# Performance work log

Measured on AMD Instinct MI355X. Metric: run time of the kernel, lower is better.

## Reference

```python
import jax, jax.numpy as jnp
import numpy as np

D_MODEL = 768
N_HEADS = 12
HEAD = 64
B, T = 2, 2048


def setup_inputs() -> dict:
    key = jax.random.key(0)
    k1, k2, k3 = jax.random.split(key, 3)
    x = jax.random.normal(k1, (B, T, D_MODEL), dtype=jnp.float32)
    W1 = jax.random.normal(k2, (3 * D_MODEL, D_MODEL), dtype=jnp.float32) * (1.0 / np.sqrt(D_MODEL))
    b1 = jnp.zeros((3 * D_MODEL,), dtype=jnp.float32)
    W2 = jax.random.normal(k3, (D_MODEL, D_MODEL), dtype=jnp.float32) * (1.0 / np.sqrt(D_MODEL))
    b2 = jnp.zeros((D_MODEL,), dtype=jnp.float32)
    return {"x": x, "W1": W1, "b1": b1, "W2": W2, "b2": b2}


def reference(x, W1, b1, W2, b2):
    Bx, Tx, C = x.shape
    qkv = jnp.einsum('btc,fc->btf', x, W1) + b1            # (B,T,3C)
    q, k, v = jnp.split(qkv, 3, axis=-1)
    # (B,T,H,Dh) -> (B,H,T,Dh)
    q = q.reshape(Bx, Tx, N_HEADS, HEAD).transpose(0, 2, 1, 3)
    k = k.reshape(Bx, Tx, N_HEADS, HEAD).transpose(0, 2, 1, 3)
    v = v.reshape(Bx, Tx, N_HEADS, HEAD).transpose(0, 2, 1, 3)
    scale = 1.0 / np.sqrt(HEAD)
    scores = jnp.einsum('bhqd,bhkd->bhqk', q, k) * scale   # (B,H,T,T)
    causal = jnp.tril(jnp.ones((Tx, Tx), dtype=bool))
    scores = jnp.where(causal, scores, jnp.finfo(scores.dtype).min)
    attn = jax.nn.softmax(scores, axis=-1)
    o = jnp.einsum('bhqk,bhkd->bhqd', attn, v)             # (B,H,T,Dh)
    o = o.transpose(0, 2, 1, 3).reshape(Bx, Tx, C)
    return jnp.einsum('btc,fc->btf', o, W2) + b2
```

## Files before the change

### kernel.cpp

```cpp
#include <hip/hip_runtime.h>


typedef float f32x4 __attribute__((ext_vector_type(4)));
typedef __bf16 bf16x8 __attribute__((ext_vector_type(8)));
typedef unsigned int u32x4 __attribute__((ext_vector_type(4)));

#define D_MODEL 768
#define F3 2304
#define NHEADS 12
#define HEAD 64
#define BB 2
#define TT 2048
#define MROWS (BB*TT)
#define KDIM 768
#define LOG2E 1.44269504f
#define NX (MROWS*D_MODEL)
#define NW1 (F3*KDIM)
#define NW2 (D_MODEL*KDIM)
#define NHT 16
#define NOF (BB*NHEADS*NHT*64*64)
#define NLF (BB*NHEADS*NHT*64)

__device__ __forceinline__ unsigned short f2bf(float f) {
    unsigned int u = __float_as_uint(f);
    u += 0x7fffu + ((u >> 16) & 1u);
    return (unsigned short)(u >> 16);
}
__device__ __forceinline__ unsigned int pack2bf(float a, float b) {
    unsigned int ua = __float_as_uint(a), ub = __float_as_uint(b);
    ua += 0x7fffu + ((ua >> 16) & 1u);
    ub += 0x7fffu + ((ub >> 16) & 1u);
    return (ua >> 16) | (ub & 0xffff0000u);
}

__device__ __forceinline__ void async_copy16(unsigned short* lds, const unsigned short* g) {
    __builtin_amdgcn_global_load_lds(
        (const __attribute__((address_space(1))) unsigned int*)(const void*)g,
        (__attribute__((address_space(3))) unsigned int*)(void*)lds,
        16, 0, 0);
}

__global__ void prep(const float* __restrict__ x, const float* __restrict__ W1,
                     const float* __restrict__ W2, unsigned short* __restrict__ xb,
                     unsigned short* __restrict__ w1b, unsigned short* __restrict__ w2b) {
    const int i4 = (blockIdx.x * blockDim.x + threadIdx.x) * 4;
    const float* src; unsigned short* dst; int off;
    if (i4 < NX)                  { src = x;  dst = xb;  off = i4; }
    else if (i4 < NX + NW1)       { src = W1; dst = w1b; off = i4 - NX; }
    else if (i4 < NX + NW1 + NW2) { src = W2; dst = w2b; off = i4 - NX - NW1; }
    else return;
    float4 v = *(const float4*)(src + off);
    uint2 o;
    o.x = pack2bf(v.x, v.y);
    o.y = pack2bf(v.z, v.w);
    *(uint2*)(dst + off) = o;
}

__global__ __launch_bounds__(256, 4) void gemm1(
    const unsigned short* __restrict__ A, const unsigned short* __restrict__ Bw,
    const float* __restrict__ bias, int K,
    unsigned short* __restrict__ Qb, unsigned short* __restrict__ Kb,
    unsigned short* __restrict__ VT)
{
    __shared__ unsigned short As[128*64];
    __shared__ unsigned short Bs[96*64];
    const int tid  = threadIdx.x;
    const int wave = tid >> 6;
    const int lane = tid & 63;
    const int quad = lane >> 4;
    const int l16  = lane & 15;

    const int F   = blockIdx.x;
    const int xcd = F & 7;
    const int idx = F >> 3;
    const int bm  = (xcd & 3) * 8 + (idx & 7);
    const int bn  = (xcd >> 2) * 12 + (idx >> 3);
    const int m0  = bm * 128;
    const int n0  = bn * 96;
    const int seg = bn >> 3;

    const int wm = (wave >> 1) * 64;
    const int wn = (wave & 1) * 48;

    f32x4 acc[4][3] = {};

    const unsigned short* Ablk = A + (size_t)m0 * K;
    const unsigned short* Bblk = Bw + (size_t)n0 * K;
    const int srow = tid >> 3;
    const int scol = ((tid & 7) ^ (srow & 7)) * 8;

    for (int k0 = 0; k0 < K; k0 += 64) {
        #pragma unroll
        for (int r = 0; r < 4; ++r)
            async_copy16(As + r*2048 + tid*8,
                         Ablk + (size_t)(r*32 + srow) * K + k0 + scol);
        #pragma unroll
        for (int r = 0; r < 3; ++r)
            async_copy16(Bs + r*2048 + tid*8,
                         Bblk + (size_t)(r*32 + srow) * K + k0 + scol);
        asm volatile("s_waitcnt vmcnt(0)" ::: "memory");
        __syncthreads();

        #pragma unroll
        for (int kc2 = 0; kc2 < 2; ++kc2) {
            const int pos = ((kc2*4 + quad) ^ (l16 & 7)) * 8;
            bf16x8 a[4], b[3];
            #pragma unroll
            for (int i = 0; i < 4; ++i)
                a[i] = *(const bf16x8*)(As + (wm + i*16 + l16)*64 + pos);
            #pragma unroll
            for (int j = 0; j < 3; ++j)
                b[j] = *(const bf16x8*)(Bs + (wn + j*16 + l16)*64 + pos);
            #pragma unroll
            for (int i = 0; i < 4; ++i)
                #pragma unroll
                for (int j = 0; j < 3; ++j)
                    acc[i][j] = __builtin_amdgcn_mfma_f32_16x16x32_bf16(a[i], b[j], acc[i][j], 0, 0, 0);
        }
        __syncthreads();
    }

    if (seg < 2) {
        #pragma unroll
        for (int j = 0; j < 3; ++j) {
            const int n = n0 + wn + j*16 + l16;
            const float bv = bias[n];
            const int f = n - seg * 768;
            const int h = f >> 6, d = f & 63;
            #pragma unroll
            for (int i = 0; i < 4; ++i)
                #pragma unroll
                for (int r = 0; r < 4; ++r) {
                    const int m = m0 + wm + i*16 + quad*4 + r;
                    const int b = m >> 11, t = m & 2047;
                    const size_t idxq = (((size_t)(b*NHEADS + h)) * TT + t) * HEAD + d;
                    const float v = acc[i][j][r] + bv;
                    if (seg == 0) Qb[idxq] = f2bf(v * (0.125f * LOG2E));
                    else          Kb[idxq] = f2bf(v);
                }
        }
    } else {
        #pragma unroll
        for (int j = 0; j < 3; ++j) {
            const int n = n0 + wn + j*16 + l16;
            const float bv = bias[n];
            const int f = n - 1536;
            const int h = f >> 6, d = f & 63;
            #pragma unroll
            for (int i = 0; i < 4; ++i) {
                const int m = m0 + wm + i*16 + quad*4;
                const int b = m >> 11, t = m & 2047;
                uint2 pk;
                pk.x = pack2bf(acc[i][j][0] + bv, acc[i][j][1] + bv);
                pk.y = pack2bf(acc[i][j][2] + bv, acc[i][j][3] + bv);
                *(uint2*)(VT + ((size_t)(b*NHEADS + h) * HEAD + d) * TT + t) = pk;
            }
        }
    }
}

__global__ __launch_bounds__(256, 4) void gemm2(
    const unsigned short* __restrict__ A, const unsigned short* __restrict__ Bw,
    const float* __restrict__ bias, int K, float* __restrict__ Cout)
{
    __shared__ unsigned short As[64*64];
    __shared__ unsigned short Bs[96*64];
    const int tid  = threadIdx.x;
    const int wave = tid >> 6;
    const int lane = tid & 63;
    const int quad = lane >> 4;
    const int l16  = lane & 15;

    const int F   = blockIdx.x;
    const int xcd = F & 7;
    const int idx = F >> 3;
    const int m0  = ((xcd & 3) * 16 + (idx & 15)) * 64;
    const int n0  = ((xcd >> 2) * 4 + (idx >> 4)) * 96;

    const int wm = (wave >> 1) * 32;
    const int wn = (wave & 1) * 48;

    f32x4 acc[2][3] = {};

    const unsigned short* Ablk = A + (size_t)m0 * K;
    const unsigned short* Bblk = Bw + (size_t)n0 * K;
    const int srow = tid >> 3;
    const int scol = ((tid & 7) ^ (srow & 7)) * 8;

    for (int k0 = 0; k0 < K; k0 += 64) {
        #pragma unroll
        for (int r = 0; r < 2; ++r)
            async_copy16(As + r*2048 + tid*8,
                         Ablk + (size_t)(r*32 + srow) * K + k0 + scol);
        #pragma unroll
        for (int r = 0; r < 3; ++r)
            async_copy16(Bs + r*2048 + tid*8,
                         Bblk + (size_t)(r*32 + srow) * K + k0 + scol);
        asm volatile("s_waitcnt vmcnt(0)" ::: "memory");
        __syncthreads();

        #pragma unroll
        for (int kc2 = 0; kc2 < 2; ++kc2) {
            const int pos = ((kc2*4 + quad) ^ (l16 & 7)) * 8;
            bf16x8 a[2], b[3];
            #pragma unroll
            for (int i = 0; i < 2; ++i)
                a[i] = *(const bf16x8*)(As + (wm + i*16 + l16)*64 + pos);
            #pragma unroll
            for (int j = 0; j < 3; ++j)
                b[j] = *(const bf16x8*)(Bs + (wn + j*16 + l16)*64 + pos);
            #pragma unroll
            for (int i = 0; i < 2; ++i)
                #pragma unroll
                for (int j = 0; j < 3; ++j)
                    acc[i][j] = __builtin_amdgcn_mfma_f32_16x16x32_bf16(a[i], b[j], acc[i][j], 0, 0, 0);
        }
        __syncthreads();
    }

    #pragma unroll
    for (int j = 0; j < 3; ++j) {
        const int n = n0 + wn + j*16 + l16;
        const float bv = bias[n];
        #pragma unroll
        for (int i = 0; i < 2; ++i)
            #pragma unroll
            for (int r = 0; r < 4; ++r) {
                const int m = m0 + wm + i*16 + quad*4 + r;
                Cout[(size_t)m * D_MODEL + n] = acc[i][j][r] + bv;
            }
    }
}

__global__ __launch_bounds__(256, 4) void attn(
    const unsigned short* __restrict__ Qb, const unsigned short* __restrict__ Kb,
    const unsigned short* __restrict__ VT, unsigned short* __restrict__ Ob,
    float* __restrict__ OfA, float* __restrict__ OfB,
    float* __restrict__ LfA, float* __restrict__ LfB)
{
    __shared__ unsigned short Ks[128*64];
    __shared__ unsigned short Vt[64*128];

    const int tid  = threadIdx.x;
    const int wave = tid >> 6;
    const int lane = tid & 63;
    const int quad = lane >> 4;
    const int l16  = lane & 15;

    const int F    = blockIdx.y * 32 + blockIdx.x;
    const int xcd  = F & 7;
    const int slot = F >> 3;
    const int bh   = xcd * 3 + (slot >> 5);
    const int j    = slot & 31;

    const int i    = j & 15;
    const bool isA = (j < 16);
    const int half = i >> 1;
    const int split = 8 - half;
    const size_t hbase = (size_t)bh * TT * HEAD;

    const int krow = tid >> 3;
    const int kchunk = ((tid & 7) ^ (krow & 7)) * 8;
    const int vrow = tid >> 4;
    const int vchunk = ((tid & 15) ^ vrow) * 8;

    const int nseg = isA ? 2 : 1;
    for (int segi = 0; segi < nseg; ++segi) {
        int qt, kb, ke; bool full;
        if (isA) {
            if (segi == 0) { qt = i;      kb = 0;     ke = half + 1;  full = true;  }
            else           { qt = 31 - i; kb = 0;     ke = split;     full = false; }
        } else             { qt = 31 - i; kb = split; ke = 16 - half; full = false; }
        const bool domask = (ke == (qt >> 1) + 1);
        const int qg = qt*64 + wave*16 + l16;

        bf16x8 qreg[2];
        {
            const unsigned short* qp = Qb + hbase + (size_t)qg * HEAD + quad*8;
            qreg[0] = *(const bf16x8*)(qp);
            qreg[1] = *(const bf16x8*)(qp + 32);
        }

        f32x4 oacc[4] = {};
        float lst = 0.f;

        for (int kt = kb; kt < ke; ++kt) {
            __syncthreads();

            const unsigned short* ksrc = Kb + hbase + (size_t)kt * 128 * HEAD;
            #pragma unroll
            for (int ii = 0; ii < 4; ++ii)
                async_copy16(Ks + ii*2048 + tid*8,
                             ksrc + (size_t)(ii*32 + krow) * 64 + kchunk);
            #pragma unroll
            for (int ii = 0; ii < 4; ++ii)
                async_copy16(Vt + ii*2048 + tid*8,
                             VT + hbase + (size_t)(ii*16 + vrow) * TT + kt*128 + vchunk);
            asm volatile("s_waitcnt vmcnt(0)" ::: "memory");
            __syncthreads();

            f32x4 s[8] = {};
            #pragma unroll
            for (int kc2 = 0; kc2 < 2; ++kc2) {
                bf16x8 bq = qreg[kc2];
                const int pos = ((kc2*4 + quad) ^ (l16 & 7)) * 8;
                #pragma unroll
                for (int nt = 0; nt < 8; ++nt) {
                    bf16x8 ak = *(const bf16x8*)(Ks + (nt*16 + l16)*64 + pos);
                    s[nt] = __builtin_amdgcn_mfma_f32_16x16x32_bf16(ak, bq, s[nt], 0, 0, 0);
                }
            }

            if (domask && kt == ke - 1) {
                const int kq = kt*128 + quad*4;
                #pragma unroll
                for (int nt = 0; nt < 8; ++nt)
                    #pragma unroll
                    for (int r = 0; r < 4; ++r)
                        if (kq + nt*16 + r > qg) s[nt][r] = -1e30f;
            }

            float rsum = 0.f;
            uint2 pck[8];
            #pragma unroll
            for (int nt = 0; nt < 8; ++nt) {
                const float p0 = exp2f(s[nt][0]);
                const float p1 = exp2f(s[nt][1]);
                const float p2 = exp2f(s[nt][2]);
                const float p3 = exp2f(s[nt][3]);
                rsum += (p0 + p1) + (p2 + p3);
                pck[nt].x = (__float_as_uint(p0) >> 16) | (__float_as_uint(p1) & 0xffff0000u);
                pck[nt].y = (__float_as_uint(p2) >> 16) | (__float_as_uint(p3) & 0xffff0000u);
            }
            rsum += __shfl_xor(rsum, 16);
            rsum += __shfl_xor(rsum, 32);
            lst += rsum;

            #pragma unroll
            for (int kc = 0; kc < 4; ++kc) {
                u32x4 pw = {pck[2*kc].x, pck[2*kc].y, pck[2*kc+1].x, pck[2*kc+1].y};
                bf16x8 ap = __builtin_bit_cast(bf16x8, pw);
                const int g1 = 4*kc + (quad >> 1);
                const int c1 = ((g1     ^ l16) * 8) + (quad & 1) * 4;
                const int c2 = (((g1+2) ^ l16) * 8) + (quad & 1) * 4;
                #pragma unroll
                for (int dt = 0; dt < 4; ++dt) {
                    const unsigned short* vr = Vt + (dt*16 + l16)*128;
                    uint2 lo = *(const uint2*)(vr + c1);
                    uint2 hi = *(const uint2*)(vr + c2);
                    u32x4 vv = {lo.x, lo.y, hi.x, hi.y};
                    bf16x8 bv = __builtin_bit_cast(bf16x8, vv);
                    oacc[dt] = __builtin_amdgcn_mfma_f32_16x16x32_bf16(ap, bv, oacc[dt], 0, 0, 0);
                }
            }
        }

        if (full) {
            const float linv = 1.0f / lst;
            float lr[4];
            #pragma unroll
            for (int r = 0; r < 4; ++r) lr[r] = __shfl(linv, quad*4 + r);
            const int b = bh / NHEADS, h = bh % NHEADS;
            #pragma unroll
            for (int r = 0; r < 4; ++r) {
                const int m = b * TT + qt*64 + wave*16 + quad*4 + r;
                #pragma unroll
                for (int dt = 0; dt < 4; ++dt)
                    Ob[(size_t)m * D_MODEL + h*HEAD + dt*16 + l16] = f2bf(oacc[dt][r] * lr[r]);
            }
        } else {
            const int qtl = qt - 16;
            float* op = (isA ? OfA : OfB)
                        + (((size_t)(bh*NHT + qtl))*64 + wave*16)*64;
            #pragma unroll
            for (int dt = 0; dt < 4; ++dt)
                #pragma unroll
                for (int r = 0; r < 4; ++r)
                    op[(quad*4 + r)*64 + dt*16 + l16] = oacc[dt][r];
            if (quad == 0)
                (isA ? LfA : LfB)[((size_t)(bh*NHT + qtl))*64 + wave*16 + l16] = lst;
        }
    }
}

__global__ __launch_bounds__(256) void fixup(
    const float* __restrict__ OfA, const float* __restrict__ OfB,
    const float* __restrict__ LfA, const float* __restrict__ LfB,
    unsigned short* __restrict__ Ob)
{
    const int qtl = blockIdx.x;
    const int bh  = blockIdx.y;
    const int t   = threadIdx.x;
    const int r   = t >> 2;
    const int c0  = (t & 3) * 16;
    const size_t lidx = ((size_t)(bh*NHT + qtl))*64 + r;
    const float linv = 1.0f / (LfA[lidx] + LfB[lidx]);
    const size_t base = (((size_t)(bh*NHT + qtl))*64 + r)*64 + c0;
    const float* sa = OfA + base;
    const float* sb = OfB + base;
    const int b = bh / NHEADS, h = bh % NHEADS;
    const int m = b*TT + (16 + qtl)*64 + r;
    unsigned short* dst = Ob + (size_t)m * D_MODEL + h*HEAD + c0;
    uint4 o0, o1;
    {
        f32x4 a0 = *(const f32x4*)(sa);      f32x4 b0 = *(const f32x4*)(sb);
        f32x4 a1 = *(const f32x4*)(sa + 4);  f32x4 b1 = *(const f32x4*)(sb + 4);
        f32x4 v0 = a0 + b0, v1 = a1 + b1;
        o0.x = pack2bf(v0[0]*linv, v0[1]*linv);
        o0.y = pack2bf(v0[2]*linv, v0[3]*linv);
        o0.z = pack2bf(v1[0]*linv, v1[1]*linv);
        o0.w = pack2bf(v1[2]*linv, v1[3]*linv);
    }
    {
        f32x4 a2 = *(const f32x4*)(sa + 8);  f32x4 b2 = *(const f32x4*)(sb + 8);
        f32x4 a3 = *(const f32x4*)(sa + 12); f32x4 b3 = *(const f32x4*)(sb + 12);
        f32x4 v2 = a2 + b2, v3 = a3 + b3;
        o1.x = pack2bf(v2[0]*linv, v2[1]*linv);
        o1.y = pack2bf(v2[2]*linv, v2[3]*linv);
        o1.z = pack2bf(v3[0]*linv, v3[1]*linv);
        o1.w = pack2bf(v3[2]*linv, v3[3]*linv);
    }
    *(uint4*)(dst)     = o0;
    *(uint4*)(dst + 8) = o1;
}

extern "C" void kernel_launch(void* const* d_in, const int* in_sizes, int n_in,
                              void* d_out, int out_size, void* d_ws, size_t ws_size,
                              hipStream_t stream) {
    const float* x  = (const float*)d_in[0];
    const float* W1 = (const float*)d_in[1];
    const float* b1 = (const float*)d_in[2];
    const float* W2 = (const float*)d_in[3];
    const float* b2 = (const float*)d_in[4];
    float* out = (float*)d_out;

    unsigned short* ws = (unsigned short*)d_ws;
    unsigned short* xb  = ws;
    unsigned short* w1b = xb  + (size_t)NX;
    unsigned short* w2b = w1b + (size_t)NW1;
    unsigned short* Qb  = w2b + (size_t)NW2;
    unsigned short* Kb  = Qb + (size_t)BB*NHEADS*TT*HEAD;
    unsigned short* VT  = Kb + (size_t)BB*NHEADS*TT*HEAD;
    unsigned short* Ob  = VT + (size_t)BB*NHEADS*TT*HEAD;
    float* OfA = (float*)(Ob + (size_t)NX);
    float* OfB = OfA + (size_t)NOF;
    float* LfA = OfB + (size_t)NOF;
    float* LfB = LfA + (size_t)NLF;

    prep<<<((NX + NW1 + NW2)/4 + 255)/256, 256, 0, stream>>>(
        x, W1, W2, xb, w1b, w2b);

    gemm1<<<768, 256, 0, stream>>>(
        xb, w1b, b1, KDIM, Qb, Kb, VT);

    attn<<<dim3(32, BB*NHEADS), 256, 0, stream>>>(
        Qb, Kb, VT, Ob, OfA, OfB, LfA, LfB);

    fixup<<<dim3(NHT, BB*NHEADS), 256, 0, stream>>>(OfA, OfB, LfA, LfB, Ob);

    gemm2<<<512, 256, 0, stream>>>(
        Ob, w2b, b2, KDIM, out);
}
```

Measured before the change: 145.3 us.

## Double-buffer K tiles and split waits so V load overlaps QK compute

Makes the K shared-memory tile double-buffered, prefetching the next K tile while the current one is processed. The single full vmcnt(0) wait is split: QK^T starts once K is ready, and V is waited on only before the PV MFMAs. This hides global-to-LDS latency within a block. It costs 16KB more LDS per block, and launch bounds drop from 4 to 3 blocks per CU, which may reduce occupancy-based latency hiding. The manual vmcnt counts and raw s_barrier calls must match the issue order exactly.

```diff
diff --git a/kernel.cpp b/kernel.cpp
--- a/kernel.cpp
+++ b/kernel.cpp
@@ -232,13 +232,13 @@
     }
 }
 
-__global__ __launch_bounds__(256, 4) void attn(
+__global__ __launch_bounds__(256, 3) void attn(
     const unsigned short* __restrict__ Qb, const unsigned short* __restrict__ Kb,
     const unsigned short* __restrict__ VT, unsigned short* __restrict__ Ob,
     float* __restrict__ OfA, float* __restrict__ OfB,
     float* __restrict__ LfA, float* __restrict__ LfB)
 {
-    __shared__ unsigned short Ks[128*64];
+    __shared__ unsigned short Ks[2][128*64];
     __shared__ unsigned short Vt[64*128];
 
     const int tid  = threadIdx.x;
@@ -281,23 +281,39 @@
             qreg[1] = *(const bf16x8*)(qp + 32);
         }
 
+        if (segi) __syncthreads();
+
+        {
+            const unsigned short* ksrc = Kb + hbase + (size_t)kb * 128 * HEAD;
+            #pragma unroll
+            for (int ii = 0; ii < 4; ++ii)
+                async_copy16(&Ks[0][ii*2048 + tid*8],
+                             ksrc + (size_t)(ii*32 + krow) * 64 + kchunk);
+        }
+        int cur = 0;
+
         f32x4 oacc[4] = {};
         float lst = 0.f;
 
         for (int kt = kb; kt < ke; ++kt) {
-            __syncthreads();
-
-            const unsigned short* ksrc = Kb + hbase + (size_t)kt * 128 * HEAD;
-            #pragma unroll
-            for (int ii = 0; ii < 4; ++ii)
-                async_copy16(Ks + ii*2048 + tid*8,
-                             ksrc + (size_t)(ii*32 + krow) * 64 + kchunk);
+            __builtin_amdgcn_s_barrier();
+
             #pragma unroll
             for (int ii = 0; ii < 4; ++ii)
                 async_copy16(Vt + ii*2048 + tid*8,
                              VT + hbase + (size_t)(ii*16 + vrow) * TT + kt*128 + vchunk);
-            asm volatile("s_waitcnt vmcnt(0)" ::: "memory");
-            __syncthreads();
+            const bool more = (kt + 1 < ke);
+            if (more) {
+                const unsigned short* knxt = Kb + hbase + (size_t)(kt+1) * 128 * HEAD;
+                #pragma unroll
+                for (int ii = 0; ii < 4; ++ii)
+                    async_copy16(&Ks[cur^1][ii*2048 + tid*8],
+                                 knxt + (size_t)(ii*32 + krow) * 64 + kchunk);
+                asm volatile("s_waitcnt vmcnt(8)" ::: "memory");
+            } else {
+                asm volatile("s_waitcnt vmcnt(4)" ::: "memory");
+            }
+            __builtin_amdgcn_s_barrier();
 
             f32x4 s[8] = {};
             #pragma unroll
@@ -306,7 +322,7 @@
                 const int pos = ((kc2*4 + quad) ^ (l16 & 7)) * 8;
                 #pragma unroll
                 for (int nt = 0; nt < 8; ++nt) {
-                    bf16x8 ak = *(const bf16x8*)(Ks + (nt*16 + l16)*64 + pos);
+                    bf16x8 ak = *(const bf16x8*)(&Ks[cur][(nt*16 + l16)*64 + pos]);
                     s[nt] = __builtin_amdgcn_mfma_f32_16x16x32_bf16(ak, bq, s[nt], 0, 0, 0);
                 }
             }
@@ -336,6 +352,10 @@
             rsum += __shfl_xor(rsum, 32);
             lst += rsum;
 
+            if (more) asm volatile("s_waitcnt vmcnt(4)" ::: "memory");
+            else      asm volatile("s_waitcnt vmcnt(0)" ::: "memory");
+            __builtin_amdgcn_s_barrier();
+
             #pragma unroll
             for (int kc = 0; kc < 4; ++kc) {
                 u32x4 pw = {pck[2*kc].x, pck[2*kc].y, pck[2*kc+1].x, pck[2*kc+1].y};
@@ -353,6 +373,7 @@
                     oacc[dt] = __builtin_amdgcn_mfma_f32_16x16x32_bf16(ap, bv, oacc[dt], 0, 0, 0);
                 }
             }
+            cur ^= 1;
         }
 
         if (full) {
```

After: 146.9 us. About the same (+1.1%).

## Switch attention to 32x32x16 MFMA with split-K waves and LDS reduction

Applied to the files above, without the earlier changes.

Rewrites the attention inner loop to use 32x32x16 bf16 MFMA tiles. Waves are split into two query halves and two key halves, so each wave computes a 32x64 slice, and the partial outputs and row sums of the two key halves are combined through LDS at the end. The larger tiles are meant to cut LDS traffic per FLOP and use the higher-throughput MFMA shape. In exchange it adds an extra reduction pass and syncs, uses more registers (occupancy hint lowered from 4 to 3), and depends on pack2bf being defined elsewhere.

```diff
diff --git a/kernel.cpp b/kernel.cpp
--- a/kernel.cpp
+++ b/kernel.cpp
@@ -2,6 +2,7 @@
 
 
 typedef float f32x4 __attribute__((ext_vector_type(4)));
+typedef float f32x16 __attribute__((ext_vector_type(16)));
 typedef __bf16 bf16x8 __attribute__((ext_vector_type(8)));
 typedef unsigned int u32x4 __attribute__((ext_vector_type(4)));
 
@@ -232,7 +233,7 @@
     }
 }
 
-__global__ __launch_bounds__(256, 4) void attn(
+__global__ __launch_bounds__(256, 3) void attn(
     const unsigned short* __restrict__ Qb, const unsigned short* __restrict__ Kb,
     const unsigned short* __restrict__ VT, unsigned short* __restrict__ Ob,
     float* __restrict__ OfA, float* __restrict__ OfB,
@@ -244,8 +245,10 @@
     const int tid  = threadIdx.x;
     const int wave = tid >> 6;
     const int lane = tid & 63;
-    const int quad = lane >> 4;
-    const int l16  = lane & 15;
+    const int hi   = lane >> 5;
+    const int l32  = lane & 31;
+    const int qh   = wave & 1;
+    const int kh   = wave >> 1;
 
     const int F    = blockIdx.y * 32 + blockIdx.x;
     const int xcd  = F & 7;
@@ -272,16 +275,14 @@
             else           { qt = 31 - i; kb = 0;     ke = split;     full = false; }
         } else             { qt = 31 - i; kb = split; ke = 16 - half; full = false; }
         const bool domask = (ke == (qt >> 1) + 1);
-        const int qg = qt*64 + wave*16 + l16;
-
-        bf16x8 qreg[2];
-        {
-            const unsigned short* qp = Qb + hbase + (size_t)qg * HEAD + quad*8;
-            qreg[0] = *(const bf16x8*)(qp);
-            qreg[1] = *(const bf16x8*)(qp + 32);
-        }
-
-        f32x4 oacc[4] = {};
+        const int qg = qt*64 + qh*32 + l32;
+
+        bf16x8 qreg[4];
+        #pragma unroll
+        for (int dk = 0; dk < 4; ++dk)
+            qreg[dk] = *(const bf16x8*)(Qb + hbase + (size_t)qg * HEAD + dk*16 + hi*8);
+
+        f32x16 oacc[2] = {};
         float lst = 0.f;
 
         for (int kt = kb; kt < ke; ++kt) {
@@ -299,86 +300,114 @@
             asm volatile("s_waitcnt vmcnt(0)" ::: "memory");
             __syncthreads();
 
-            f32x4 s[8] = {};
-            #pragma unroll
-            for (int kc2 = 0; kc2 < 2; ++kc2) {
-                bf16x8 bq = qreg[kc2];
-                const int pos = ((kc2*4 + quad) ^ (l16 & 7)) * 8;
-                #pragma unroll
-                for (int nt = 0; nt < 8; ++nt) {
-                    bf16x8 ak = *(const bf16x8*)(Ks + (nt*16 + l16)*64 + pos);
-                    s[nt] = __builtin_amdgcn_mfma_f32_16x16x32_bf16(ak, bq, s[nt], 0, 0, 0);
+            f32x16 s[2] = {};
+            #pragma unroll
+            for (int dk = 0; dk < 4; ++dk) {
+                const bf16x8 bq = qreg[dk];
+                #pragma unroll
+                for (int nt = 0; nt < 2; ++nt) {
+                    const int r = kh*64 + nt*32 + l32;
+                    const bf16x8 ak = *(const bf16x8*)(Ks + r*64 + (((dk*2 + hi) ^ (r & 7)) * 8));
+                    s[nt] = __builtin_amdgcn_mfma_f32_32x32x16_bf16(ak, bq, s[nt], 0, 0, 0);
                 }
             }
 
             if (domask && kt == ke - 1) {
-                const int kq = kt*128 + quad*4;
-                #pragma unroll
-                for (int nt = 0; nt < 8; ++nt)
+                const int kbase = kt*128 + kh*64;
+                #pragma unroll
+                for (int nt = 0; nt < 2; ++nt)
                     #pragma unroll
-                    for (int r = 0; r < 4; ++r)
-                        if (kq + nt*16 + r > qg) s[nt][r] = -1e30f;
+                    for (int e = 0; e < 16; ++e) {
+                        const int kk = kbase + nt*32 + (e & 3) + 8*(e >> 2) + 4*hi;
+                        if (kk > qg) s[nt][e] = -1e30f;
+                    }
             }
 
             float rsum = 0.f;
-            uint2 pck[8];
-            #pragma unroll
-            for (int nt = 0; nt < 8; ++nt) {
-                const float p0 = exp2f(s[nt][0]);
-                const float p1 = exp2f(s[nt][1]);
-                const float p2 = exp2f(s[nt][2]);
-                const float p3 = exp2f(s[nt][3]);
-                rsum += (p0 + p1) + (p2 + p3);
-                pck[nt].x = (__float_as_uint(p0) >> 16) | (__float_as_uint(p1) & 0xffff0000u);
-                pck[nt].y = (__float_as_uint(p2) >> 16) | (__float_as_uint(p3) & 0xffff0000u);
-            }
-            rsum += __shfl_xor(rsum, 16);
+            unsigned int w[2][8];
+            #pragma unroll
+            for (int nt = 0; nt < 2; ++nt)
+                #pragma unroll
+                for (int e2 = 0; e2 < 8; ++e2) {
+                    const float p0 = exp2f(s[nt][2*e2]);
+                    const float p1 = exp2f(s[nt][2*e2 + 1]);
+                    rsum += p0 + p1;
+                    w[nt][e2] = pack2bf(p0, p1);
+                }
             rsum += __shfl_xor(rsum, 32);
             lst += rsum;
 
             #pragma unroll
             for (int kc = 0; kc < 4; ++kc) {
-                u32x4 pw = {pck[2*kc].x, pck[2*kc].y, pck[2*kc+1].x, pck[2*kc+1].y};
-                bf16x8 ap = __builtin_bit_cast(bf16x8, pw);
-                const int g1 = 4*kc + (quad >> 1);
-                const int c1 = ((g1     ^ l16) * 8) + (quad & 1) * 4;
-                const int c2 = (((g1+2) ^ l16) * 8) + (quad & 1) * 4;
-                #pragma unroll
-                for (int dt = 0; dt < 4; ++dt) {
-                    const unsigned short* vr = Vt + (dt*16 + l16)*128;
-                    uint2 lo = *(const uint2*)(vr + c1);
-                    uint2 hi = *(const uint2*)(vr + c2);
-                    u32x4 vv = {lo.x, lo.y, hi.x, hi.y};
-                    bf16x8 bv = __builtin_bit_cast(bf16x8, vv);
-                    oacc[dt] = __builtin_amdgcn_mfma_f32_16x16x32_bf16(ap, bv, oacc[dt], 0, 0, 0);
+                const int nt = kc >> 1, sub = kc & 1;
+                u32x4 pw = {w[nt][4*sub], w[nt][4*sub+1], w[nt][4*sub+2], w[nt][4*sub+3]};
+                const bf16x8 ap = __builtin_bit_cast(bf16x8, pw);
+                const int g0 = kh*8 + kc*2;
+                #pragma unroll
+                for (int dt = 0; dt < 2; ++dt) {
+                    const int d = dt*32 + l32;
+                    const unsigned short* vr = Vt + d*128;
+                    const uint2 lo = *(const uint2*)(vr + ((g0     ^ (d & 15)) * 8) + hi*4);
+                    const uint2 h2 = *(const uint2*)(vr + (((g0+1) ^ (d & 15)) * 8) + hi*4);
+                    u32x4 vv = {lo.x, lo.y, h2.x, h2.y};
+                    const bf16x8 av = __builtin_bit_cast(bf16x8, vv);
+                    oacc[dt] = __builtin_amdgcn_mfma_f32_32x32x16_bf16(av, ap, oacc[dt], 0, 0, 0);
                 }
             }
         }
 
-        if (full) {
-            const float linv = 1.0f / lst;
-            float lr[4];
-            #pragma unroll
-            for (int r = 0; r < 4; ++r) lr[r] = __shfl(linv, quad*4 + r);
-            const int b = bh / NHEADS, h = bh % NHEADS;
-            #pragma unroll
-            for (int r = 0; r < 4; ++r) {
-                const int m = b * TT + qt*64 + wave*16 + quad*4 + r;
-                #pragma unroll
-                for (int dt = 0; dt < 4; ++dt)
-                    Ob[(size_t)m * D_MODEL + h*HEAD + dt*16 + l16] = f2bf(oacc[dt][r] * lr[r]);
-            }
-        } else {
-            const int qtl = qt - 16;
-            float* op = (isA ? OfA : OfB)
-                        + (((size_t)(bh*NHT + qtl))*64 + wave*16)*64;
-            #pragma unroll
-            for (int dt = 0; dt < 4; ++dt)
-                #pragma unroll
-                for (int r = 0; r < 4; ++r)
-                    op[(quad*4 + r)*64 + dt*16 + l16] = oacc[dt][r];
-            if (quad == 0)
-                (isA ? LfA : LfB)[((size_t)(bh*NHT + qtl))*64 + wave*16 + l16] = lst;
+        __syncthreads();
+        {
+            float* Oc = (float*)Vt;
+            float* Lc = (float*)Ks;
+            if (kh == 1) {
+                #pragma unroll
+                for (int dt = 0; dt < 2; ++dt)
+                    #pragma unroll
+                    for (int e = 0; e < 16; ++e)
+                        Oc[qh*2048 + dt*1024 + e*64 + lane] = oacc[dt][e];
+                if (lane < 32) Lc[qh*32 + lane] = lst;
+            }
+            __syncthreads();
+            if (kh == 0) {
+                #pragma unroll
+                for (int dt = 0; dt < 2; ++dt)
+                    #pragma unroll
+                    for (int e = 0; e < 16; ++e)
+                        oacc[dt][e] += Oc[qh*2048 + dt*1024 + e*64 + lane];
+                lst += Lc[qh*32 + l32];
+
+                if (full) {
+                    const float linv = 1.0f / lst;
+                    const int b = bh / NHEADS, h = bh % NHEADS;
+                    const int m = b * TT + qg;
+                    unsigned short* dst = Ob + (size_t)m * D_MODEL + h*HEAD;
+                    #pragma unroll
+                    for (int dt = 0; dt < 2; ++dt)
+                        #pragma unroll
+                        for (int q4 = 0; q4 < 4; ++q4) {
+                            const int e = q4*4;
+                            uint2 pk;
+                            pk.x = pack2bf(oacc[dt][e]*linv,   oacc[dt][e+1]*linv);
+                            pk.y = pack2bf(oacc[dt][e+2]*linv, oacc[dt][e+3]*linv);
+                            *(uint2*)(dst + dt*32 + q4*8 + hi*4) = pk;
+                        }
+                } else {
+                    const int qtl = qt - 16;
+                    float* op = (isA ? OfA : OfB)
+                                + (((size_t)(bh*NHT + qtl))*64 + qh*32 + l32)*64;
+                    #pragma unroll
+                    for (int dt = 0; dt < 2; ++dt)
+                        #pragma unroll
+                        for (int q4 = 0; q4 < 4; ++q4) {
+                            const int e = q4*4;
+                            f32x4 v = {oacc[dt][e], oacc[dt][e+1], oacc[dt][e+2], oacc[dt][e+3]};
+                            *(f32x4*)(op + dt*32 + q4*8 + hi*4) = v;
+                        }
+                    if (lane < 32)
+                        (isA ? LfA : LfB)[((size_t)(bh*NHT + qtl))*64 + qh*32 + lane] = lst;
+                }
+            }
         }
     }
 }
```

Measured after the change: 146.9 us. About the same (+1.1%).

## Split key blocks across waves in attention and drop the split-K fixup kernel

Applied to the files above, without the earlier changes.

Restructures the attention kernel so each block handles two balanced 32-row query tiles. Each of the four waves processes a 32-key slice of every 128-key tile, and the partial outputs and row sums are combined through LDS at the end. This removes the global fp32 partial-output buffers and the separate fixup launch that the old query-split scheme needed. In exchange it adds an LDS reduction step and extra barriers, changes P rounding to round-to-nearest packing, and lowers the launch-bounds occupancy hint from 4 to 3.

```diff
diff --git a/kernel.cpp b/kernel.cpp
--- a/kernel.cpp
+++ b/kernel.cpp
@@ -17,9 +17,6 @@
 #define NX (MROWS*D_MODEL)
 #define NW1 (F3*KDIM)
 #define NW2 (D_MODEL*KDIM)
-#define NHT 16
-#define NOF (BB*NHEADS*NHT*64*64)
-#define NLF (BB*NHEADS*NHT*64)
 
 __device__ __forceinline__ unsigned short f2bf(float f) {
     unsigned int u = __float_as_uint(f);
@@ -232,11 +229,9 @@
     }
 }
 
-__global__ __launch_bounds__(256, 4) void attn(
+__global__ __launch_bounds__(256, 3) void attn(
     const unsigned short* __restrict__ Qb, const unsigned short* __restrict__ Kb,
-    const unsigned short* __restrict__ VT, unsigned short* __restrict__ Ob,
-    float* __restrict__ OfA, float* __restrict__ OfB,
-    float* __restrict__ LfA, float* __restrict__ LfB)
+    const unsigned short* __restrict__ VT, unsigned short* __restrict__ Ob)
 {
     __shared__ unsigned short Ks[128*64];
     __shared__ unsigned short Vt[64*128];
@@ -252,11 +247,6 @@
     const int slot = F >> 3;
     const int bh   = xcd * 3 + (slot >> 5);
     const int j    = slot & 31;
-
-    const int i    = j & 15;
-    const bool isA = (j < 16);
-    const int half = i >> 1;
-    const int split = 8 - half;
     const size_t hbase = (size_t)bh * TT * HEAD;
 
     const int krow = tid >> 3;
@@ -264,27 +254,24 @@
     const int vrow = tid >> 4;
     const int vchunk = ((tid & 15) ^ vrow) * 8;
 
-    const int nseg = isA ? 2 : 1;
-    for (int segi = 0; segi < nseg; ++segi) {
-        int qt, kb, ke; bool full;
-        if (isA) {
-            if (segi == 0) { qt = i;      kb = 0;     ke = half + 1;  full = true;  }
-            else           { qt = 31 - i; kb = 0;     ke = split;     full = false; }
-        } else             { qt = 31 - i; kb = split; ke = 16 - half; full = false; }
-        const bool domask = (ke == (qt >> 1) + 1);
-        const int qg = qt*64 + wave*16 + l16;
-
-        bf16x8 qreg[2];
-        {
-            const unsigned short* qp = Qb + hbase + (size_t)qg * HEAD + quad*8;
-            qreg[0] = *(const bf16x8*)(qp);
-            qreg[1] = *(const bf16x8*)(qp + 32);
-        }
-
-        f32x4 oacc[4] = {};
-        float lst = 0.f;
-
-        for (int kt = kb; kt < ke; ++kt) {
+    #pragma unroll 1
+    for (int seg = 0; seg < 2; ++seg) {
+        const int t   = seg ? (63 - j) : j;
+        const int nkt = (t >> 2) + 1;
+        const int q0  = t * 32;
+
+        bf16x8 qreg[2][2];
+        #pragma unroll
+        for (int qs = 0; qs < 2; ++qs) {
+            const unsigned short* qp = Qb + hbase + (size_t)(q0 + qs*16 + l16) * HEAD + quad*8;
+            qreg[qs][0] = *(const bf16x8*)(qp);
+            qreg[qs][1] = *(const bf16x8*)(qp + 32);
+        }
+
+        f32x4 oacc[2][4] = {};
+        float lst[2] = {0.f, 0.f};
+
+        for (int kt = 0; kt < nkt; ++kt) {
             __syncthreads();
 
             const unsigned short* ksrc = Kb + hbase + (size_t)kt * 128 * HEAD;
@@ -299,129 +286,123 @@
             asm volatile("s_waitcnt vmcnt(0)" ::: "memory");
             __syncthreads();
 
-            f32x4 s[8] = {};
+            f32x4 s[2][2] = {};
             #pragma unroll
             for (int kc2 = 0; kc2 < 2; ++kc2) {
-                bf16x8 bq = qreg[kc2];
                 const int pos = ((kc2*4 + quad) ^ (l16 & 7)) * 8;
                 #pragma unroll
-                for (int nt = 0; nt < 8; ++nt) {
-                    bf16x8 ak = *(const bf16x8*)(Ks + (nt*16 + l16)*64 + pos);
-                    s[nt] = __builtin_amdgcn_mfma_f32_16x16x32_bf16(ak, bq, s[nt], 0, 0, 0);
+                for (int n = 0; n < 2; ++n) {
+                    const bf16x8 ak = *(const bf16x8*)(Ks + (wave*32 + n*16 + l16)*64 + pos);
+                    #pragma unroll
+                    for (int qs = 0; qs < 2; ++qs)
+                        s[n][qs] = __builtin_amdgcn_mfma_f32_16x16x32_bf16(ak, qreg[qs][kc2], s[n][qs], 0, 0, 0);
                 }
             }
 
-            if (domask && kt == ke - 1) {
-                const int kq = kt*128 + quad*4;
-                #pragma unroll
-                for (int nt = 0; nt < 8; ++nt)
+            if (kt == (t >> 2)) {
+                const int kq = kt*128 + wave*32 + quad*4;
+                #pragma unroll
+                for (int n = 0; n < 2; ++n)
+                    #pragma unroll
+                    for (int qs = 0; qs < 2; ++qs)
+                        #pragma unroll
+                        for (int r = 0; r < 4; ++r)
+                            if (kq + n*16 + r > q0 + qs*16 + l16) s[n][qs][r] = -1e30f;
+            }
+
+            uint2 pck[2][2];
+            #pragma unroll
+            for (int n = 0; n < 2; ++n)
+                #pragma unroll
+                for (int qs = 0; qs < 2; ++qs) {
+                    const float p0 = exp2f(s[n][qs][0]);
+                    const float p1 = exp2f(s[n][qs][1]);
+                    const float p2 = exp2f(s[n][qs][2]);
+                    const float p3 = exp2f(s[n][qs][3]);
+                    lst[qs] += (p0 + p1) + (p2 + p3);
+                    pck[n][qs].x = pack2bf(p0, p1);
+                    pck[n][qs].y = pack2bf(p2, p3);
+                }
+
+            bf16x8 ap[2];
+            #pragma unroll
+            for (int qs = 0; qs < 2; ++qs) {
+                u32x4 pw = {pck[0][qs].x, pck[0][qs].y, pck[1][qs].x, pck[1][qs].y};
+                ap[qs] = __builtin_bit_cast(bf16x8, pw);
+            }
+            const int g1 = wave*4 + (quad >> 1);
+            #pragma unroll
+            for (int dt = 0; dt < 4; ++dt) {
+                const unsigned short* vr = Vt + (dt*16 + l16)*128;
+                const int c1 = ((g1     ^ l16) * 8) + (quad & 1) * 4;
+                const int c2 = (((g1+2) ^ l16) * 8) + (quad & 1) * 4;
+                const uint2 lo = *(const uint2*)(vr + c1);
+                const uint2 hi = *(const uint2*)(vr + c2);
+                u32x4 vv = {lo.x, lo.y, hi.x, hi.y};
+                const bf16x8 bv = __builtin_bit_cast(bf16x8, vv);
+                #pragma unroll
+                for (int qs = 0; qs < 2; ++qs)
+                    oacc[qs][dt] = __builtin_amdgcn_mfma_f32_16x16x32_bf16(ap[qs], bv, oacc[qs][dt], 0, 0, 0);
+            }
+        }
+
+        #pragma unroll
+        for (int qs = 0; qs < 2; ++qs) {
+            lst[qs] += __shfl_xor(lst[qs], 16);
+            lst[qs] += __shfl_xor(lst[qs], 32);
+        }
+
+        __syncthreads();
+        {
+            float* O1 = (float*)Ks;
+            float* O2 = (float*)Ks + 2048;
+            float* O3 = (float*)Vt;
+            float* Lb = (float*)Vt + 2048;
+            if (wave != 0) {
+                float* ob = (wave == 1) ? O1 : (wave == 2) ? O2 : O3;
+                #pragma unroll
+                for (int qs = 0; qs < 2; ++qs)
+                    #pragma unroll
+                    for (int dt = 0; dt < 4; ++dt)
+                        #pragma unroll
+                        for (int r = 0; r < 4; ++r)
+                            ob[(qs*16 + quad*4 + r)*64 + dt*16 + l16] = oacc[qs][dt][r];
+                if (lane < 16) {
+                    Lb[(wave-1)*32 + l16]      = lst[0];
+                    Lb[(wave-1)*32 + 16 + l16] = lst[1];
+                }
+            }
+            __syncthreads();
+            if (wave == 0) {
+                float linv[2], lr[2][4];
+                #pragma unroll
+                for (int qs = 0; qs < 2; ++qs) {
+                    const float lt = lst[qs] + Lb[qs*16 + l16] + Lb[32 + qs*16 + l16]
+                                             + Lb[64 + qs*16 + l16];
+                    linv[qs] = 1.0f / lt;
+                }
+                #pragma unroll
+                for (int qs = 0; qs < 2; ++qs)
                     #pragma unroll
                     for (int r = 0; r < 4; ++r)
-                        if (kq + nt*16 + r > qg) s[nt][r] = -1e30f;
-            }
-
-            float rsum = 0.f;
-            uint2 pck[8];
-            #pragma unroll
-            for (int nt = 0; nt < 8; ++nt) {
-                const float p0 = exp2f(s[nt][0]);
-                const float p1 = exp2f(s[nt][1]);
-                const float p2 = exp2f(s[nt][2]);
-                const float p3 = exp2f(s[nt][3]);
-                rsum += (p0 + p1) + (p2 + p3);
-                pck[nt].x = (__float_as_uint(p0) >> 16) | (__float_as_uint(p1) & 0xffff0000u);
-                pck[nt].y = (__float_as_uint(p2) >> 16) | (__float_as_uint(p3) & 0xffff0000u);
-            }
-            rsum += __shfl_xor(rsum, 16);
-            rsum += __shfl_xor(rsum, 32);
-            lst += rsum;
-
-            #pragma unroll
-            for (int kc = 0; kc < 4; ++kc) {
-                u32x4 pw = {pck[2*kc].x, pck[2*kc].y, pck[2*kc+1].x, pck[2*kc+1].y};
-                bf16x8 ap = __builtin_bit_cast(bf16x8, pw);
-                const int g1 = 4*kc + (quad >> 1);
-                const int c1 = ((g1     ^ l16) * 8) + (quad & 1) * 4;
-                const int c2 = (((g1+2) ^ l16) * 8) + (quad & 1) * 4;
-                #pragma unroll
-                for (int dt = 0; dt < 4; ++dt) {
-                    const unsigned short* vr = Vt + (dt*16 + l16)*128;
-                    uint2 lo = *(const uint2*)(vr + c1);
-                    uint2 hi = *(const uint2*)(vr + c2);
-                    u32x4 vv = {lo.x, lo.y, hi.x, hi.y};
-                    bf16x8 bv = __builtin_bit_cast(bf16x8, vv);
-                    oacc[dt] = __builtin_amdgcn_mfma_f32_16x16x32_bf16(ap, bv, oacc[dt], 0, 0, 0);
-                }
-            }
-        }
-
-        if (full) {
-            const float linv = 1.0f / lst;
-            float lr[4];
-            #pragma unroll
-            for (int r = 0; r < 4; ++r) lr[r] = __shfl(linv, quad*4 + r);
-            const int b = bh / NHEADS, h = bh % NHEADS;
-            #pragma unroll
-            for (int r = 0; r < 4; ++r) {
-                const int m = b * TT + qt*64 + wave*16 + quad*4 + r;
-                #pragma unroll
-                for (int dt = 0; dt < 4; ++dt)
-                    Ob[(size_t)m * D_MODEL + h*HEAD + dt*16 + l16] = f2bf(oacc[dt][r] * lr[r]);
-            }
-        } else {
-            const int qtl = qt - 16;
-            float* op = (isA ? OfA : OfB)
-                        + (((size_t)(bh*NHT + qtl))*64 + wave*16)*64;
-            #pragma unroll
-            for (int dt = 0; dt < 4; ++dt)
-                #pragma unroll
-                for (int r = 0; r < 4; ++r)
-                    op[(quad*4 + r)*64 + dt*16 + l16] = oacc[dt][r];
-            if (quad == 0)
-                (isA ? LfA : LfB)[((size_t)(bh*NHT + qtl))*64 + wave*16 + l16] = lst;
+                        lr[qs][r] = __shfl(linv[qs], quad*4 + r);
+                const int b = bh / NHEADS, h = bh % NHEADS;
+                #pragma unroll
+                for (int qs = 0; qs < 2; ++qs)
+                    #pragma unroll
+                    for (int r = 0; r < 4; ++r) {
+                        const int m = b * TT + q0 + qs*16 + quad*4 + r;
+                        unsigned short* dst = Ob + (size_t)m * D_MODEL + h*HEAD;
+                        #pragma unroll
+                        for (int dt = 0; dt < 4; ++dt) {
+                            const int idx = (qs*16 + quad*4 + r)*64 + dt*16 + l16;
+                            const float v = oacc[qs][dt][r] + O1[idx] + O2[idx] + O3[idx];
+                            dst[dt*16 + l16] = f2bf(v * lr[qs][r]);
+                        }
+                    }
+            }
         }
     }
-}
-
-__global__ __launch_bounds__(256) void fixup(
-    const float* __restrict__ OfA, const float* __restrict__ OfB,
-    const float* __restrict__ LfA, const float* __restrict__ LfB,
-    unsigned short* __restrict__ Ob)
-{
-    const int qtl = blockIdx.x;
-    const int bh  = blockIdx.y;
-    const int t   = threadIdx.x;
-    const int r   = t >> 2;
-    const int c0  = (t & 3) * 16;
-    const size_t lidx = ((size_t)(bh*NHT + qtl))*64 + r;
-    const float linv = 1.0f / (LfA[lidx] + LfB[lidx]);
-    const size_t base = (((size_t)(bh*NHT + qtl))*64 + r)*64 + c0;
-    const float* sa = OfA + base;
-    const float* sb = OfB + base;
-    const int b = bh / NHEADS, h = bh % NHEADS;
-    const int m = b*TT + (16 + qtl)*64 + r;
-    unsigned short* dst = Ob + (size_t)m * D_MODEL + h*HEAD + c0;
-    uint4 o0, o1;
-    {
-        f32x4 a0 = *(const f32x4*)(sa);      f32x4 b0 = *(const f32x4*)(sb);
-        f32x4 a1 = *(const f32x4*)(sa + 4);  f32x4 b1 = *(const f32x4*)(sb + 4);
-        f32x4 v0 = a0 + b0, v1 = a1 + b1;
-        o0.x = pack2bf(v0[0]*linv, v0[1]*linv);
-        o0.y = pack2bf(v0[2]*linv, v0[3]*linv);
-        o0.z = pack2bf(v1[0]*linv, v1[1]*linv);
-        o0.w = pack2bf(v1[2]*linv, v1[3]*linv);
-    }
-    {
-        f32x4 a2 = *(const f32x4*)(sa + 8);  f32x4 b2 = *(const f32x4*)(sb + 8);
-        f32x4 a3 = *(const f32x4*)(sa + 12); f32x4 b3 = *(const f32x4*)(sb + 12);
-        f32x4 v2 = a2 + b2, v3 = a3 + b3;
-        o1.x = pack2bf(v2[0]*linv, v2[1]*linv);
-        o1.y = pack2bf(v2[2]*linv, v2[3]*linv);
-        o1.z = pack2bf(v3[0]*linv, v3[1]*linv);
-        o1.w = pack2bf(v3[2]*linv, v3[3]*linv);
-    }
-    *(uint4*)(dst)     = o0;
-    *(uint4*)(dst + 8) = o1;
 }
 
 extern "C" void kernel_launch(void* const* d_in, const int* in_sizes, int n_in,
@@ -442,10 +423,6 @@
     unsigned short* Kb  = Qb + (size_t)BB*NHEADS*TT*HEAD;
     unsigned short* VT  = Kb + (size_t)BB*NHEADS*TT*HEAD;
     unsigned short* Ob  = VT + (size_t)BB*NHEADS*TT*HEAD;
-    float* OfA = (float*)(Ob + (size_t)NX);
-    float* OfB = OfA + (size_t)NOF;
-    float* LfA = OfB + (size_t)NOF;
-    float* LfB = LfA + (size_t)NLF;
 
     prep<<<((NX + NW1 + NW2)/4 + 255)/256, 256, 0, stream>>>(
         x, W1, W2, xb, w1b, w2b);
@@ -453,10 +430,7 @@
     gemm1<<<768, 256, 0, stream>>>(
         xb, w1b, b1, KDIM, Qb, Kb, VT);
 
-    attn<<<dim3(32, BB*NHEADS), 256, 0, stream>>>(
-        Qb, Kb, VT, Ob, OfA, OfB, LfA, LfB);
-
-    fixup<<<dim3(NHT, BB*NHEADS), 256, 0, stream>>>(OfA, OfB, LfA, LfB, Ob);
+    attn<<<dim3(32, BB*NHEADS), 256, 0, stream>>>(Qb, Kb, VT, Ob);
 
     gemm2<<<512, 256, 0, stream>>>(
         Ob, w2b, b2, KDIM, out);
```

Result: no change. 146.6 us (+0.9%).
